# Kernel tuning notes

Hardware: AMD Instinct MI355X
Metric: run time of the kernel (lower is better)

Reference implementation:

```python
import jax, jax.numpy as jnp
import numpy as np

N_NODES = 50000


def gcn_layer(x, src, dst, W, b):
    # GCNConv: out = D^{-1/2} (A + I) D^{-1/2} (x W) + b
    n = x.shape[0]
    h = x @ W  # [N, C_out]
    # degree including self-loop (count of incoming edges at dst + 1)
    deg = jnp.zeros((n,), dtype=x.dtype).at[dst].add(1.0) + 1.0
    dinv_sqrt = jax.lax.rsqrt(deg)
    norm = dinv_sqrt[src] * dinv_sqrt[dst]  # [E]
    agg = jax.ops.segment_sum(h[src] * norm[:, None], dst, num_segments=n)
    # self-loop contribution: norm_ii = 1/deg_i
    agg = agg + h * (dinv_sqrt * dinv_sqrt)[:, None]
    return agg + b


def setup_inputs() -> dict:
    key = jax.random.key(0)
    k1, k2, k3, k4, k5, k6 = jax.random.split(key, 6)
    in_c, hid_c, out_c = 128, 128, 64
    x = jax.random.normal(k1, (N_NODES, in_c), dtype=jnp.float32)
    edge_index = jax.random.randint(k2, (2, 600000), 0, N_NODES, dtype=jnp.int64)
    W1 = jax.random.normal(k3, (in_c, hid_c), dtype=jnp.float32) * (1.0 / np.sqrt(in_c))
    b1 = jnp.zeros((hid_c,), dtype=jnp.float32)
    W2 = jax.random.normal(k4, (hid_c, out_c), dtype=jnp.float32) * (1.0 / np.sqrt(hid_c))
    b2 = jnp.zeros((out_c,), dtype=jnp.float32)
    return {"x": x, "edge_index": edge_index, "W1": W1, "b1": b1, "W2": W2, "b2": b2}


def reference(x, edge_index, W1, b1, W2, b2):
    src, dst = edge_index[0], edge_index[1]
    h = gcn_layer(x, src, dst, W1, b1)
    h = jax.nn.relu(h)
    out = gcn_layer(h, src, dst, W2, b2)
    return out
```

## Files before the change

### kernel.cpp

```cpp
#include <hip/hip_runtime.h>

#define IN_C 128
#define HID_C 128
#define OUT_C 64
#define CAP 40
#define LSTR 40

typedef unsigned int uint;
typedef unsigned short ushort;
typedef __attribute__((ext_vector_type(8))) short short8;
typedef __attribute__((ext_vector_type(4))) float f32x4;

__device__ __forceinline__ float bf2f(ushort u) {
    return __uint_as_float(((uint)u) << 16);
}
__device__ __forceinline__ float bfl(uint u) {
    return __uint_as_float(u << 16);
}
__device__ __forceinline__ float bfh(uint u) {
    return __uint_as_float(u & 0xffff0000u);
}
__device__ __forceinline__ ushort f2bf(float f) {
    uint u = __float_as_uint(f);
    return (ushort)((u + 0x7fffu + ((u >> 16) & 1u)) >> 16);
}


__global__ void prep0_kernel(int* __restrict__ cursor, int n,
                             const float* __restrict__ W1, ushort* __restrict__ w1h,
                             ushort* __restrict__ w1l, const float* __restrict__ W2,
                             ushort* __restrict__ w2h, ushort* __restrict__ w2l) {
    int idx = blockIdx.x * blockDim.x + threadIdx.x;
    if (idx < n) {
        cursor[idx] = 0;
    } else if (idx < n + 128 * 128) {
        int i1 = idx - n;
        int k = i1 >> 7, c = i1 & 127;
        float w = W1[i1];
        ushort h = f2bf(w);
        ushort l = f2bf(w - bf2f(h));
        w1h[c * 128 + k] = h;
        w1l[c * 128 + k] = l;
    } else if (idx < n + 128 * 128 + 128 * 64) {
        int i2 = idx - n - 128 * 128;
        int k = i2 >> 6, c = i2 & 63;
        float w = W2[i2];
        ushort h = f2bf(w);
        ushort l = f2bf(w - bf2f(h));
        w2h[c * 128 + k] = h;
        w2l[c * 128 + k] = l;
    }
}


__global__ __launch_bounds__(256) void gemm1_edge_kernel(
    const float* __restrict__ A, const ushort* __restrict__ BTh,
    const ushort* __restrict__ BTl, ushort* __restrict__ C, int M, int gblocks,
    const int* __restrict__ src, const int* __restrict__ dst,
    int* __restrict__ cursor, int* __restrict__ csr_src, int E) {
    constexpr int BN = 128;
    constexpr int NT = BN / 16;
    __shared__ ushort sAh[64 * LSTR], sAl[64 * LSTR];
    __shared__ ushort sBh[BN * LSTR], sBl[BN * LSTR];

    const int tid = threadIdx.x;

    if (blockIdx.x >= gblocks) {
        int e = (blockIdx.x - gblocks) * 256 + tid;
        if (e < E) {
            unsigned s = (unsigned)src[e];
            unsigned d = (unsigned)dst[e];
            if (s < (unsigned)M && d < (unsigned)M) {
                int p = atomicAdd(&cursor[d], 1);
                if (p < CAP) csr_src[d * CAP + p] = (int)s;
            }
        }
        return;
    }

    const int w = tid >> 6;
    const int lane = tid & 63;
    const int m = lane & 15;
    const int quad = lane >> 4;
    const int r0 = blockIdx.x * 64;

    f32x4 acc[NT];
#pragma unroll
    for (int t = 0; t < NT; ++t) acc[t] = (f32x4){0.f, 0.f, 0.f, 0.f};

    for (int k0 = 0; k0 < 128; k0 += 32) {
#pragma unroll
        for (int it = 0; it < 2; ++it) {
            int idx = tid + it * 256;
            int row = idx >> 3;
            int c4 = idx & 7;
            int grow = r0 + row;
            float4 v = make_float4(0.f, 0.f, 0.f, 0.f);
            if (grow < M) v = *(const float4*)&A[(size_t)grow * 128 + k0 + c4 * 4];
            ushort h0 = f2bf(v.x), h1 = f2bf(v.y), h2 = f2bf(v.z), h3 = f2bf(v.w);
            ushort l0 = f2bf(v.x - bf2f(h0)), l1 = f2bf(v.y - bf2f(h1));
            ushort l2 = f2bf(v.z - bf2f(h2)), l3 = f2bf(v.w - bf2f(h3));
            *(ushort4*)&sAh[row * LSTR + c4 * 4] = make_ushort4(h0, h1, h2, h3);
            *(ushort4*)&sAl[row * LSTR + c4 * 4] = make_ushort4(l0, l1, l2, l3);
        }
        for (int idx = tid; idx < BN * 4; idx += 256) {
            int row = idx >> 2;
            int c = idx & 3;
            *(uint4*)&sBh[row * LSTR + c * 8] = *(const uint4*)&BTh[row * 128 + k0 + c * 8];
            *(uint4*)&sBl[row * LSTR + c * 8] = *(const uint4*)&BTl[row * 128 + k0 + c * 8];
        }
        __syncthreads();

        short8 ah = *(const short8*)&sAh[(w * 16 + m) * LSTR + quad * 8];
        short8 al = *(const short8*)&sAl[(w * 16 + m) * LSTR + quad * 8];
#pragma unroll
        for (int t = 0; t < NT; ++t) {
            short8 bh = *(const short8*)&sBh[(t * 16 + m) * LSTR + quad * 8];
            short8 bl = *(const short8*)&sBl[(t * 16 + m) * LSTR + quad * 8];
            acc[t] = __builtin_amdgcn_mfma_f32_16x16x32_bf16(ah, bh, acc[t], 0, 0, 0);
            acc[t] = __builtin_amdgcn_mfma_f32_16x16x32_bf16(al, bh, acc[t], 0, 0, 0);
            acc[t] = __builtin_amdgcn_mfma_f32_16x16x32_bf16(ah, bl, acc[t], 0, 0, 0);
        }
        __syncthreads();
    }

#pragma unroll
    for (int t = 0; t < NT; ++t) {
#pragma unroll
        for (int r = 0; r < 4; ++r) {
            int row = r0 + w * 16 + quad * 4 + r;
            if (row < M) C[(size_t)row * BN + t * 16 + m] = f2bf(acc[t][r]);
        }
    }
}


#define ACC8(v, nn)                                     \
    {                                                   \
        a0 += (nn) * bfl((v).x); a1 += (nn) * bfh((v).x); \
        a2 += (nn) * bfl((v).y); a3 += (nn) * bfh((v).y); \
        a4 += (nn) * bfl((v).z); a5 += (nn) * bfh((v).z); \
        a6 += (nn) * bfl((v).w); a7 += (nn) * bfh((v).w); \
    }


__global__ __launch_bounds__(256) void agg_gemm2_kernel(
    const uint4* __restrict__ hx, const int* __restrict__ csr_src,
    const int* __restrict__ degs, const float* __restrict__ bias,
    const ushort* __restrict__ BTh, const ushort* __restrict__ BTl,
    ushort* __restrict__ C, int n) {
    __shared__ ushort sAf[4][32][LSTR];
    __shared__ ushort sBh[64 * LSTR], sBl[64 * LSTR];

    const int tid = threadIdx.x;
    const int w = tid >> 6;
    const int lane = tid & 63;
    const int q4 = lane >> 4;
    const int c16 = lane & 15;
    const int r0 = blockIdx.x * 32;

    int nd = 0, t0 = 0, t1 = 0, t2 = 0;
    {
        int node = r0 + w * 8 + q4;
        bool valid = node < n;
        nd = valid ? degs[node] : 0;
        size_t base = (size_t)node * CAP;
        t0 = valid ? csr_src[base + c16] : 0;
        t1 = valid ? csr_src[base + 16 + c16] : 0;
        t2 = (valid && c16 < 8) ? csr_src[base + 32 + c16] : 0;
    }

    for (int g = 0; g < 2; ++g) {
        const int lrow = w * 8 + g * 4 + q4;
        const int node = r0 + lrow;
        const bool valid = node < n;
        const int cnt = min(nd, CAP);
        const float degf = (float)(cnt + 1);
        const float dinv = rsqrtf(degf);
        int es0 = (c16 < cnt) ? t0 : 0;
        int es1 = (16 + c16 < cnt) ? t1 : 0;
        int es2 = (32 + c16 < cnt) ? t2 : 0;
        int d0 = degs[es0];
        int d1 = degs[es1];
        int d2 = degs[es2];
        uint4 sv = make_uint4(0u, 0u, 0u, 0u);
        if (valid) sv = hx[(size_t)node * 16 + c16];
        int nd_n = 0, t0n = 0, t1n = 0, t2n = 0;
        if (g + 1 < 2) {
            int node_n = r0 + w * 8 + (g + 1) * 4 + q4;
            bool vn = node_n < n;
            nd_n = vn ? degs[node_n] : 0;
            size_t base_n = (size_t)node_n * CAP;
            t0n = vn ? csr_src[base_n + c16] : 0;
            t1n = vn ? csr_src[base_n + 16 + c16] : 0;
            t2n = (vn && c16 < 8) ? csr_src[base_n + 32 + c16] : 0;
        }
        float en0 = (c16 < cnt) ? rsqrtf((float)(d0 + 1)) * dinv : 0.f;
        float en1 = (16 + c16 < cnt) ? rsqrtf((float)(d1 + 1)) * dinv : 0.f;
        float en2 = (32 + c16 < cnt) ? rsqrtf((float)(d2 + 1)) * dinv : 0.f;
        int cm = cnt;
        cm = max(cm, __shfl_xor(cm, 16));
        cm = max(cm, __shfl_xor(cm, 32));

        float a0 = 0.f, a1 = 0.f, a2 = 0.f, a3 = 0.f;
        float a4 = 0.f, a5 = 0.f, a6 = 0.f, a7 = 0.f;

        auto EDGE = [&](int kk, int& s, float& wt) {
            if (kk < 16) {
                s = __shfl(es0, (q4 << 4) + kk);
                wt = __shfl(en0, (q4 << 4) + kk);
            } else if (kk < 32) {
                s = __shfl(es1, (q4 << 4) + kk - 16);
                wt = __shfl(en1, (q4 << 4) + kk - 16);
            } else {
                s = __shfl(es2, (q4 << 4) + kk - 32);
                wt = __shfl(en2, (q4 << 4) + kk - 32);
            }
        };

        int k = 0;
        for (; k + 2 <= cm; k += 2) {
            int sA; float nA; EDGE(k, sA, nA);
            int sB; float nB; EDGE(k + 1, sB, nB);
            uint4 vA = hx[(size_t)sA * 16 + c16];
            uint4 vB = hx[(size_t)sB * 16 + c16];
            ACC8(vA, nA);
            ACC8(vB, nB);
        }
        if (k < cm) {
            int sA; float nA; EDGE(k, sA, nA);
            uint4 vA = hx[(size_t)sA * 16 + c16];
            ACC8(vA, nA);
        }

        float sn = 1.0f / degf;
        const float4* b4 = (const float4*)bias;
        float4 bA = b4[2 * c16], bB = b4[2 * c16 + 1];
        float o0 = fmaxf(a0 + bfl(sv.x) * sn + bA.x, 0.f);
        float o1 = fmaxf(a1 + bfh(sv.x) * sn + bA.y, 0.f);
        float o2 = fmaxf(a2 + bfl(sv.y) * sn + bA.z, 0.f);
        float o3 = fmaxf(a3 + bfh(sv.y) * sn + bA.w, 0.f);
        float o4 = fmaxf(a4 + bfl(sv.z) * sn + bB.x, 0.f);
        float o5 = fmaxf(a5 + bfh(sv.z) * sn + bB.y, 0.f);
        float o6 = fmaxf(a6 + bfl(sv.w) * sn + bB.z, 0.f);
        float o7 = fmaxf(a7 + bfh(sv.w) * sn + bB.w, 0.f);
        uint4 u;
        u.x = (uint)f2bf(o0) | ((uint)f2bf(o1) << 16);
        u.y = (uint)f2bf(o2) | ((uint)f2bf(o3) << 16);
        u.z = (uint)f2bf(o4) | ((uint)f2bf(o5) << 16);
        u.w = (uint)f2bf(o6) | ((uint)f2bf(o7) << 16);
        *(uint4*)&sAf[c16 >> 2][lrow][(c16 & 3) * 8] = u;

        nd = nd_n; t0 = t0n; t1 = t1n; t2 = t2n;
    }

    const int wm = w >> 1;
    const int wn = w & 1;
    f32x4 acc[2];
#pragma unroll
    for (int t = 0; t < 2; ++t) acc[t] = (f32x4){0.f, 0.f, 0.f, 0.f};

    for (int k0 = 0; k0 < 128; k0 += 32) {
        {
            int row = tid >> 2;
            int c = tid & 3;
            *(uint4*)&sBh[row * LSTR + c * 8] = *(const uint4*)&BTh[row * 128 + k0 + c * 8];
            *(uint4*)&sBl[row * LSTR + c * 8] = *(const uint4*)&BTl[row * 128 + k0 + c * 8];
        }
        __syncthreads();

        short8 ah = *(const short8*)&sAf[k0 >> 5][wm * 16 + c16][q4 * 8];
#pragma unroll
        for (int t = 0; t < 2; ++t) {
            int tt = wn * 2 + t;
            short8 bh = *(const short8*)&sBh[(tt * 16 + c16) * LSTR + q4 * 8];
            short8 bl = *(const short8*)&sBl[(tt * 16 + c16) * LSTR + q4 * 8];
            acc[t] = __builtin_amdgcn_mfma_f32_16x16x32_bf16(ah, bh, acc[t], 0, 0, 0);
            acc[t] = __builtin_amdgcn_mfma_f32_16x16x32_bf16(ah, bl, acc[t], 0, 0, 0);
        }
        __syncthreads();
    }

#pragma unroll
    for (int t = 0; t < 2; ++t) {
#pragma unroll
        for (int r = 0; r < 4; ++r) {
            int row = r0 + wm * 16 + q4 * 4 + r;
            if (row < n) C[(size_t)row * 64 + (wn * 2 + t) * 16 + c16] = f2bf(acc[t][r]);
        }
    }
}


__global__ __launch_bounds__(256) void agg64_kernel(
    const uint4* __restrict__ hx, const int* __restrict__ csr_src,
    const int* __restrict__ degs, const float* __restrict__ bias,
    float* __restrict__ out, int n) {
    int node = blockIdx.x * 4 + (threadIdx.x >> 6);
    if (node >= n) return;
    int lane = threadIdx.x & 63;
    int oct = lane >> 3;
    int q = lane & 7;
    int cnt = min(degs[node], CAP);
    float degf = (float)(cnt + 1);
    float dinv_d = rsqrtf(degf);
    int start = node * CAP;
    float a0 = 0.f, a1 = 0.f, a2 = 0.f, a3 = 0.f;
    float a4 = 0.f, a5 = 0.f, a6 = 0.f, a7 = 0.f;

    if (cnt > 0) {
        int es = (lane < cnt) ? csr_src[start + lane] : 0;
        int cs = (lane < cnt) ? degs[es] : 0;
        float en = rsqrtf((float)(cs + 1)) * dinv_d;
        int j = 0;
        for (; j + 16 <= cnt; j += 16) {
            int sA = __shfl(es, j + oct);
            float nA = __shfl(en, j + oct);
            int sB = __shfl(es, j + 8 + oct);
            float nB = __shfl(en, j + 8 + oct);
            uint4 vA = hx[(size_t)sA * 8 + q];
            uint4 vB = hx[(size_t)sB * 8 + q];
            ACC8(vA, nA);
            ACC8(vB, nB);
        }
        if (j < cnt) {
            int k0 = j + oct;
            int s0 = __shfl(es, k0);
            float n0 = __shfl(en, k0);
            n0 = (k0 < cnt) ? n0 : 0.f;
            uint4 v0 = hx[(size_t)s0 * 8 + q];
            ACC8(v0, n0);
            if (j + 8 < cnt) {
                int k1 = j + 8 + oct;
                int s1 = __shfl(es, k1);
                float n1 = __shfl(en, k1);
                n1 = (k1 < cnt) ? n1 : 0.f;
                uint4 v1 = hx[(size_t)s1 * 8 + q];
                ACC8(v1, n1);
            }
        }
    }

#pragma unroll
    for (int d = 8; d <= 32; d <<= 1) {
        a0 += __shfl_xor(a0, d); a1 += __shfl_xor(a1, d);
        a2 += __shfl_xor(a2, d); a3 += __shfl_xor(a3, d);
        a4 += __shfl_xor(a4, d); a5 += __shfl_xor(a5, d);
        a6 += __shfl_xor(a6, d); a7 += __shfl_xor(a7, d);
    }
    if (oct == 0) {
        uint4 sv = hx[(size_t)node * 8 + q];
        float sn = 1.0f / degf;
        const float4* b4 = (const float4*)bias;
        float4 bA = b4[2 * q], bB = b4[2 * q + 1];
        float4 oA, oB;
        oA.x = a0 + bfl(sv.x) * sn + bA.x;
        oA.y = a1 + bfh(sv.x) * sn + bA.y;
        oA.z = a2 + bfl(sv.y) * sn + bA.z;
        oA.w = a3 + bfh(sv.y) * sn + bA.w;
        oB.x = a4 + bfl(sv.z) * sn + bB.x;
        oB.y = a5 + bfh(sv.z) * sn + bB.y;
        oB.z = a6 + bfl(sv.w) * sn + bB.z;
        oB.w = a7 + bfh(sv.w) * sn + bB.w;
        float4* o4 = (float4*)out;
        o4[(size_t)node * 16 + 2 * q] = oA;
        o4[(size_t)node * 16 + 2 * q + 1] = oB;
    }
}


extern "C" void kernel_launch(void* const* d_in, const int* in_sizes, int n_in,
                              void* d_out, int out_size, void* d_ws, size_t ws_size,
                              hipStream_t stream) {
    (void)n_in; (void)out_size; (void)ws_size;
    const float* x  = (const float*)d_in[0];
    const int*   ei = (const int*)d_in[1];
    const float* W1 = (const float*)d_in[2];
    const float* b1 = (const float*)d_in[3];
    const float* W2 = (const float*)d_in[4];
    const float* b2 = (const float*)d_in[5];
    float* out = (float*)d_out;

    const int n = in_sizes[0] / IN_C;
    const int E = in_sizes[1] / 2;
    const int* src = ei;
    const int* dst = ei + E;

    char* ws = (char*)d_ws;
    size_t off = 0;
    auto alloc = [&](size_t bytes) -> void* {
        void* p = ws + off;
        off += (bytes + 1023) & ~(size_t)1023;
        return p;
    };

    ushort* w1h     = (ushort*)alloc(128 * 128 * 2);
    ushort* w1l     = (ushort*)alloc(128 * 128 * 2);
    ushort* w2h     = (ushort*)alloc(64 * 128 * 2);
    ushort* w2l     = (ushort*)alloc(64 * 128 * 2);
    int*    cursor  = (int*)   alloc((size_t)n * 4);
    int*    csr_src = (int*)   alloc((size_t)n * CAP * 4);
    ushort* h1      = (ushort*)alloc((size_t)n * HID_C * 2);
    ushort* h2      = (ushort*)alloc((size_t)n * HID_C * 2);

    const int gblocks = (n + 63) / 64;
    const int EB = (E + 255) / 256;
    const int fblocks = (n + 31) / 32;
    const int ablocks = (n + 3) / 4;

    prep0_kernel<<<(n + 128 * 128 + 128 * 64 + 255) / 256, 256, 0, stream>>>(
        cursor, n, W1, w1h, w1l, W2, w2h, w2l);
    gemm1_edge_kernel<<<gblocks + EB, 256, 0, stream>>>(x, w1h, w1l, h1, n, gblocks,
                                                        src, dst, cursor, csr_src, E);
    agg_gemm2_kernel<<<fblocks, 256, 0, stream>>>((const uint4*)h1, csr_src, cursor,
                                                  b1, w2h, w2l, h2, n);
    agg64_kernel<<<ablocks, 256, 0, stream>>>((const uint4*)h2, csr_src, cursor,
                                              b2, out, n);
}
```

Measured before the change: 168.7 us.

## Map one node per 8-lane group in agg64 and keep GEMM2 B in registers

The final 64-channel aggregation kernel now assigns eight nodes per wavefront, one per 8-lane group, with each group walking its own edge list. Each lane preloads up to five edge indices and normalization weights, and weights are fetched by shuffle. This replaces the one-node-per-wave scheme, which left lanes idle when degree was low and needed a cross-lane reduction at the end. Separately, agg_gemm2 loads the W2 hi/lo fragments straight from global memory into registers, dropping the shared-memory staging and three of its four barriers, at the cost of more register pressure. In the aggregation kernel, groups in a wave iterate to the maximum degree among its eight nodes, so some lanes do wasted loads with zero weight.

```diff
diff --git a/kernel.cpp b/kernel.cpp
--- a/kernel.cpp
+++ b/kernel.cpp
@@ -150,7 +150,6 @@
     const ushort* __restrict__ BTh, const ushort* __restrict__ BTl,
     ushort* __restrict__ C, int n) {
     __shared__ ushort sAf[4][32][LSTR];
-    __shared__ ushort sBh[64 * LSTR], sBl[64 * LSTR];
 
     const int tid = threadIdx.x;
     const int w = tid >> 6;
@@ -256,29 +255,32 @@
 
     const int wm = w >> 1;
     const int wn = w & 1;
+
+    short8 rbh[4][2], rbl[4][2];
+#pragma unroll
+    for (int k0x = 0; k0x < 4; ++k0x) {
+#pragma unroll
+        for (int t = 0; t < 2; ++t) {
+            int row = (wn * 2 + t) * 16 + c16;
+            rbh[k0x][t] = *(const short8*)&BTh[(size_t)row * 128 + k0x * 32 + q4 * 8];
+            rbl[k0x][t] = *(const short8*)&BTl[(size_t)row * 128 + k0x * 32 + q4 * 8];
+        }
+    }
+
+    __syncthreads();
+
     f32x4 acc[2];
 #pragma unroll
     for (int t = 0; t < 2; ++t) acc[t] = (f32x4){0.f, 0.f, 0.f, 0.f};
 
-    for (int k0 = 0; k0 < 128; k0 += 32) {
-        {
-            int row = tid >> 2;
-            int c = tid & 3;
-            *(uint4*)&sBh[row * LSTR + c * 8] = *(const uint4*)&BTh[row * 128 + k0 + c * 8];
-            *(uint4*)&sBl[row * LSTR + c * 8] = *(const uint4*)&BTl[row * 128 + k0 + c * 8];
-        }
-        __syncthreads();
-
-        short8 ah = *(const short8*)&sAf[k0 >> 5][wm * 16 + c16][q4 * 8];
+#pragma unroll
+    for (int k0x = 0; k0x < 4; ++k0x) {
+        short8 ah = *(const short8*)&sAf[k0x][wm * 16 + c16][q4 * 8];
 #pragma unroll
         for (int t = 0; t < 2; ++t) {
-            int tt = wn * 2 + t;
-            short8 bh = *(const short8*)&sBh[(tt * 16 + c16) * LSTR + q4 * 8];
-            short8 bl = *(const short8*)&sBl[(tt * 16 + c16) * LSTR + q4 * 8];
-            acc[t] = __builtin_amdgcn_mfma_f32_16x16x32_bf16(ah, bh, acc[t], 0, 0, 0);
-            acc[t] = __builtin_amdgcn_mfma_f32_16x16x32_bf16(ah, bl, acc[t], 0, 0, 0);
-        }
-        __syncthreads();
+            acc[t] = __builtin_amdgcn_mfma_f32_16x16x32_bf16(ah, rbh[k0x][t], acc[t], 0, 0, 0);
+            acc[t] = __builtin_amdgcn_mfma_f32_16x16x32_bf16(ah, rbl[k0x][t], acc[t], 0, 0, 0);
+        }
     }
 
 #pragma unroll
@@ -296,61 +298,67 @@
     const uint4* __restrict__ hx, const int* __restrict__ csr_src,
     const int* __restrict__ degs, const float* __restrict__ bias,
     float* __restrict__ out, int n) {
-    int node = blockIdx.x * 4 + (threadIdx.x >> 6);
-    if (node >= n) return;
-    int lane = threadIdx.x & 63;
-    int oct = lane >> 3;
-    int q = lane & 7;
-    int cnt = min(degs[node], CAP);
-    float degf = (float)(cnt + 1);
-    float dinv_d = rsqrtf(degf);
-    int start = node * CAP;
+    const int w = threadIdx.x >> 6;
+    const int lane = threadIdx.x & 63;
+    const int g = lane >> 3;
+    const int q = lane & 7;
+    const int node = blockIdx.x * 32 + w * 8 + g;
+    const bool valid = node < n;
+
+    int nd = valid ? degs[node] : 0;
+    const int cnt = min(nd, CAP);
+    const float dinv = rsqrtf((float)(cnt + 1));
+    const size_t base = (size_t)node * CAP;
+
+    int t0 = (valid && q < cnt) ? csr_src[base + q] : 0;
+    int t1 = (valid && 8 + q < cnt) ? csr_src[base + 8 + q] : 0;
+    int t2 = (valid && 16 + q < cnt) ? csr_src[base + 16 + q] : 0;
+    int t3 = (valid && 24 + q < cnt) ? csr_src[base + 24 + q] : 0;
+    int t4 = (valid && 32 + q < cnt) ? csr_src[base + 32 + q] : 0;
+    int d0 = degs[t0], d1 = degs[t1], d2 = degs[t2], d3 = degs[t3], d4 = degs[t4];
+    uint4 sv = make_uint4(0u, 0u, 0u, 0u);
+    if (valid) sv = hx[(size_t)node * 8 + q];
+
+    float e0 = (q < cnt) ? rsqrtf((float)(d0 + 1)) * dinv : 0.f;
+    float e1 = (8 + q < cnt) ? rsqrtf((float)(d1 + 1)) * dinv : 0.f;
+    float e2 = (16 + q < cnt) ? rsqrtf((float)(d2 + 1)) * dinv : 0.f;
+    float e3 = (24 + q < cnt) ? rsqrtf((float)(d3 + 1)) * dinv : 0.f;
+    float e4 = (32 + q < cnt) ? rsqrtf((float)(d4 + 1)) * dinv : 0.f;
+
+    int cm = cnt;
+    cm = max(cm, __shfl_xor(cm, 8));
+    cm = max(cm, __shfl_xor(cm, 16));
+    cm = max(cm, __shfl_xor(cm, 32));
+
     float a0 = 0.f, a1 = 0.f, a2 = 0.f, a3 = 0.f;
     float a4 = 0.f, a5 = 0.f, a6 = 0.f, a7 = 0.f;
 
-    if (cnt > 0) {
-        int es = (lane < cnt) ? csr_src[start + lane] : 0;
-        int cs = (lane < cnt) ? degs[es] : 0;
-        float en = rsqrtf((float)(cs + 1)) * dinv_d;
-        int j = 0;
-        for (; j + 16 <= cnt; j += 16) {
-            int sA = __shfl(es, j + oct);
-            float nA = __shfl(en, j + oct);
-            int sB = __shfl(es, j + 8 + oct);
-            float nB = __shfl(en, j + 8 + oct);
-            uint4 vA = hx[(size_t)sA * 8 + q];
-            uint4 vB = hx[(size_t)sB * 8 + q];
-            ACC8(vA, nA);
-            ACC8(vB, nB);
-        }
-        if (j < cnt) {
-            int k0 = j + oct;
-            int s0 = __shfl(es, k0);
-            float n0 = __shfl(en, k0);
-            n0 = (k0 < cnt) ? n0 : 0.f;
-            uint4 v0 = hx[(size_t)s0 * 8 + q];
-            ACC8(v0, n0);
-            if (j + 8 < cnt) {
-                int k1 = j + 8 + oct;
-                int s1 = __shfl(es, k1);
-                float n1 = __shfl(en, k1);
-                n1 = (k1 < cnt) ? n1 : 0.f;
-                uint4 v1 = hx[(size_t)s1 * 8 + q];
-                ACC8(v1, n1);
-            }
-        }
-    }
-
-#pragma unroll
-    for (int d = 8; d <= 32; d <<= 1) {
-        a0 += __shfl_xor(a0, d); a1 += __shfl_xor(a1, d);
-        a2 += __shfl_xor(a2, d); a3 += __shfl_xor(a3, d);
-        a4 += __shfl_xor(a4, d); a5 += __shfl_xor(a5, d);
-        a6 += __shfl_xor(a6, d); a7 += __shfl_xor(a7, d);
-    }
-    if (oct == 0) {
-        uint4 sv = hx[(size_t)node * 8 + q];
-        float sn = 1.0f / degf;
+    auto EDGE = [&](int kk, int& s, float& wt) {
+        int sl = (g << 3) + (kk & 7);
+        if (kk < 8)       { s = __shfl(t0, sl); wt = __shfl(e0, sl); }
+        else if (kk < 16) { s = __shfl(t1, sl); wt = __shfl(e1, sl); }
+        else if (kk < 24) { s = __shfl(t2, sl); wt = __shfl(e2, sl); }
+        else if (kk < 32) { s = __shfl(t3, sl); wt = __shfl(e3, sl); }
+        else              { s = __shfl(t4, sl); wt = __shfl(e4, sl); }
+    };
+
+    int k = 0;
+    for (; k + 2 <= cm; k += 2) {
+        int sA; float nA; EDGE(k, sA, nA);
+        int sB; float nB; EDGE(k + 1, sB, nB);
+        uint4 vA = hx[(size_t)sA * 8 + q];
+        uint4 vB = hx[(size_t)sB * 8 + q];
+        ACC8(vA, nA);
+        ACC8(vB, nB);
+    }
+    if (k < cm) {
+        int sA; float nA; EDGE(k, sA, nA);
+        uint4 vA = hx[(size_t)sA * 8 + q];
+        ACC8(vA, nA);
+    }
+
+    if (valid) {
+        float sn = dinv * dinv;
         const float4* b4 = (const float4*)bias;
         float4 bA = b4[2 * q], bB = b4[2 * q + 1];
         float4 oA, oB;
@@ -406,7 +414,6 @@
     const int gblocks = (n + 63) / 64;
     const int EB = (E + 255) / 256;
     const int fblocks = (n + 31) / 32;
-    const int ablocks = (n + 3) / 4;
 
     prep0_kernel<<<(n + 128 * 128 + 128 * 64 + 255) / 256, 256, 0, stream>>>(
         cursor, n, W1, w1h, w1l, W2, w2h, w2l);
@@ -414,6 +421,6 @@
                                                         src, dst, cursor, csr_src, E);
     agg_gemm2_kernel<<<fblocks, 256, 0, stream>>>((const uint4*)h1, csr_src, cursor,
                                                   b1, w2h, w2l, h2, n);
-    agg64_kernel<<<ablocks, 256, 0, stream>>>((const uint4*)h2, csr_src, cursor,
+    agg64_kernel<<<fblocks, 256, 0, stream>>>((const uint4*)h2, csr_src, cursor,
                                               b2, out, n);
 }
```

Measured after the change: 170.6 us. About the same (+1.1%).
